# Kernel optimization log

Measured on AMD Instinct MI355X. Metric: run time of the kernel, lower is better.

## Reference

```python
import jax, jax.numpy as jnp
import numpy as np

VOCAB, EMB, HID, LAYERS = 23, 16, 256, 8


def _lstm_layer(xseq, Wih, Whh, bih, bhh):
    # xseq: [B,T,D_in]; Wih: [4H,D_in]; Whh: [4H,H]; biases: [4H]
    B = xseq.shape[0]
    H = Whh.shape[1]
    # precompute input contribution to gates for all timesteps
    xg = jnp.einsum('btd,gd->btg', xseq, Wih) + bih + bhh  # [B,T,4H]
    xg = jnp.swapaxes(xg, 0, 1)  # [T,B,4H] for scan

    def step(carry, g_in):
        h, c = carry
        g = g_in + h @ Whh.T  # [B,4H]
        i, f, gg, o = jnp.split(g, 4, axis=-1)  # PyTorch gate order i,f,g,o
        i = jax.nn.sigmoid(i)
        f = jax.nn.sigmoid(f)
        gg = jnp.tanh(gg)
        o = jax.nn.sigmoid(o)
        c = f * c + i * gg
        h = o * jnp.tanh(c)
        return (h, c), h

    h0 = jnp.zeros((B, H), xseq.dtype)
    c0 = jnp.zeros((B, H), xseq.dtype)
    (_, _), hs = jax.lax.scan(step, (h0, c0), xg)
    return jnp.swapaxes(hs, 0, 1)  # [B,T,H]


def setup_inputs() -> dict:
    key = jax.random.key(0)
    ks = jax.random.split(key, 8)
    B, T = 64, 512
    s_e = 1.0 / np.sqrt(HID)
    x = jax.random.randint(ks[0], (B, T), 0, VOCAB)
    emb = jax.random.normal(ks[1], (VOCAB, EMB), jnp.float32)
    W_ih0 = jax.random.uniform(ks[2], (4 * HID, EMB), jnp.float32, -s_e, s_e)
    W_ih_rest = jax.random.uniform(ks[3], (LAYERS - 1, 4 * HID, HID), jnp.float32, -s_e, s_e)
    W_hh = jax.random.uniform(ks[4], (LAYERS, 4 * HID, HID), jnp.float32, -s_e, s_e)
    b_ih = jax.random.uniform(ks[5], (LAYERS, 4 * HID), jnp.float32, -s_e, s_e)
    b_hh = jax.random.uniform(ks[6], (LAYERS, 4 * HID), jnp.float32, -s_e, s_e)
    fc_w = jax.random.uniform(ks[7], (VOCAB, HID), jnp.float32, -s_e, s_e)
    fc_b = jnp.zeros((VOCAB,), jnp.float32)
    return {"x": x, "emb": emb, "W_ih0": W_ih0, "W_ih_rest": W_ih_rest,
            "W_hh": W_hh, "b_ih": b_ih, "b_hh": b_hh, "fc_w": fc_w, "fc_b": fc_b}


def reference(x, emb, W_ih0, W_ih_rest, W_hh, b_ih, b_hh, fc_w, fc_b):
    h = emb[x]  # [B,T,EMB]
    h = _lstm_layer(h, W_ih0, W_hh[0], b_ih[0], b_hh[0])
    for l in range(1, LAYERS):
        h = _lstm_layer(h, W_ih_rest[l - 1], W_hh[l], b_ih[l], b_hh[l])
    return h @ fc_w.T + fc_b  # [B,T,VOCAB]
```

## Files before the change

### kernel.cpp

```cpp
#include <hip/hip_runtime.h>
#include <cstdint>
#include <cstddef>

#define BB   64
#define TT   512
#define HH   256
#define G4   1024
#define NL   8
#define NW   32
#define HPW  8
#define NR   32

typedef _Float16 half8 __attribute__((ext_vector_type(8)));
typedef float   floatx4 __attribute__((ext_vector_type(4)));

__device__ __forceinline__ float sigm(float v)   { return 1.0f / (1.0f + __expf(-v)); }
__device__ __forceinline__ float tanh_f(float v) { return 1.0f - 2.0f / (__expf(2.0f * v) + 1.0f); }

__device__ __forceinline__ void gload8(half8& d, const _Float16* p) {
  asm volatile("global_load_dwordx4 %0, %1, off sc0 sc1"
               : "=v"(d) : "v"(p) : "memory");
}
__device__ __forceinline__ void gstore8(const _Float16* p, half8 d) {
  asm volatile("global_store_dwordx4 %0, %1, off sc0 sc1"
               :: "v"(p), "v"(d) : "memory");
}
__device__ __forceinline__ void wait_vm0() {
  asm volatile("s_waitcnt vmcnt(0)" ::: "memory");
}

#define TSTRIDE ((size_t)32 * BB * 8)
#define LSTRIDE ((size_t)TT * TSTRIDE)

__global__ void build_xg0(const float* __restrict__ emb, const float* __restrict__ Wih0,
                          float* __restrict__ table) {
  int i = blockIdx.x * 256 + threadIdx.x;
  if (i >= 23 * G4) return;
  int v = i >> 10, n = i & (G4 - 1);
  float a = 0.f;
#pragma unroll
  for (int e = 0; e < 16; ++e) a += emb[v * 16 + e] * Wih0[n * 16 + e];
  table[i] = a;
}

__global__ __launch_bounds__(256, 1) void lstm_pipeline(
    const int*   __restrict__ x,
    const float* __restrict__ Wih_rest,
    const float* __restrict__ Whh,
    const float* __restrict__ bih,
    const float* __restrict__ bhh,
    const float* __restrict__ xg0t,
    _Float16* __restrict__ hseq,
    int* __restrict__ flags)
{
  const int l   = blockIdx.x & 7;
  const int w   = blockIdx.x >> 3;
  const int tid = threadIdx.x;
  const int lane = tid & 63;
  const int p    = tid >> 6;
  const int bb   = tid & 63;

  __shared__ __align__(16) _Float16 wlds[64 * NR * 8];
  __shared__ float  glds[BB * 33];
  __shared__ __align__(16) _Float16 hl[BB * 8];
  __shared__ float  blds[NR];
  __shared__ float  tlds[23 * NR];

  for (int idx = tid; idx < 64 * NR; idx += 256) {
    int kc = idx >> 5;
    int n  = idx & 31;
    int g = n >> 3, jl = n & 7;
    int gr = g * 256 + w * HPW + jl;
    float v[8];
    if (kc < 32) {
      if (l == 0) { for (int j = 0; j < 8; ++j) v[j] = 0.f; }
      else {
        const float* src = Wih_rest + ((size_t)(l - 1) * G4 + gr) * HH + kc * 8;
        for (int j = 0; j < 8; ++j) v[j] = src[j];
      }
    } else {
      const float* src = Whh + ((size_t)l * G4 + gr) * HH + (kc - 32) * 8;
      for (int j = 0; j < 8; ++j) v[j] = src[j];
    }
    _Float16* dst = wlds + (size_t)idx * 8;
    for (int j = 0; j < 8; ++j) dst[j] = (_Float16)v[j];
  }
  if (tid < NR) {
    int g = tid >> 3, jl = tid & 7;
    int gr = g * 256 + w * HPW + jl;
    blds[tid] = bih[l * G4 + gr] + bhh[l * G4 + gr];
  }
  if (l == 0) {
    for (int idx = tid; idx < 23 * NR; idx += 256) {
      int v = idx >> 5, n = idx & 31;
      int g = n >> 3, jl = n & 7;
      tlds[idx] = xg0t[v * G4 + g * 256 + w * HPW + jl];
    }
  }
  __syncthreads();

  float c0 = 0.f, c1 = 0.f;

  const int arow = p * 16 + (lane & 15);
  const int kq   = lane >> 4;
  const int n0   = lane & 15;
  const int n1   = 16 + n0;

  const _Float16* hin  = hseq + (size_t)(l > 0 ? l - 1 : 0) * LSTRIDE;
  _Float16*       hrec = hseq + (size_t)l * LSTRIDE;
  int* flg_in  = flags + (l > 0 ? (l - 1) * TT : 0);
  int* flg_own = flags + l * TT;

  for (int t = 0; t < TT; ++t) {
    floatx4 acc0 = {0.f, 0.f, 0.f, 0.f};
    floatx4 acc1 = {0.f, 0.f, 0.f, 0.f};

    if (tid == 0 && l > 0) {
      while (__hip_atomic_load(flg_in + t, __ATOMIC_RELAXED, __HIP_MEMORY_SCOPE_AGENT) < NW)
        __builtin_amdgcn_s_sleep(1);
    }
    __syncthreads();

    if (l > 0) {
      const _Float16* ain = hin + (size_t)t * TSTRIDE;
      half8 a[8];
#pragma unroll
      for (int kt = 0; kt < 8; ++kt) {
        int kc = kt * 4 + kq;
        gload8(a[kt], ain + ((size_t)(kc * 64 + arow) << 3));
      }
      wait_vm0();
#pragma unroll
      for (int kt = 0; kt < 8; ++kt) {
        int kc = kt * 4 + kq;
        half8 w0 = *(const half8*)(wlds + ((kc * 32 + n0) << 3));
        half8 w1 = *(const half8*)(wlds + ((kc * 32 + n1) << 3));
        acc0 = __builtin_amdgcn_mfma_f32_16x16x32_f16(a[kt], w0, acc0, 0, 0, 0);
        acc1 = __builtin_amdgcn_mfma_f32_16x16x32_f16(a[kt], w1, acc1, 0, 0, 0);
      }
    }

    if (tid == 0 && t > 0) {
      while (__hip_atomic_load(flg_own + (t - 1), __ATOMIC_RELAXED, __HIP_MEMORY_SCOPE_AGENT) < NW)
        __builtin_amdgcn_s_sleep(1);
    }
    __syncthreads();

    if (t > 0) {
      const _Float16* ain = hrec + (size_t)(t - 1) * TSTRIDE;
      half8 a[8];
#pragma unroll
      for (int kt = 0; kt < 8; ++kt) {
        int kc = kt * 4 + kq;
        gload8(a[kt], ain + ((size_t)(kc * 64 + arow) << 3));
      }
      wait_vm0();
#pragma unroll
      for (int kt = 0; kt < 8; ++kt) {
        int kc = kt * 4 + kq;
        half8 w0 = *(const half8*)(wlds + (((32 + kc) * 32 + n0) << 3));
        half8 w1 = *(const half8*)(wlds + (((32 + kc) * 32 + n1) << 3));
        acc0 = __builtin_amdgcn_mfma_f32_16x16x32_f16(a[kt], w0, acc0, 0, 0, 0);
        acc1 = __builtin_amdgcn_mfma_f32_16x16x32_f16(a[kt], w1, acc1, 0, 0, 0);
      }
    }

    {
      int rbase = p * 16 + kq * 4;
#pragma unroll
      for (int r = 0; r < 4; ++r) {
        glds[(rbase + r) * 33 + n0]      = acc0[r];
        glds[(rbase + r) * 33 + 16 + n0] = acc1[r];
      }
    }
    __syncthreads();

    {
      int xv = 0;
      if (l == 0) xv = x[bb * TT + t];
      float h0, h1;
#pragma unroll
      for (int q = 0; q < 2; ++q) {
        int j = 2 * p + q;
        float gi = glds[bb * 33 + j]      + blds[j];
        float gf = glds[bb * 33 + 8 + j]  + blds[8 + j];
        float gg = glds[bb * 33 + 16 + j] + blds[16 + j];
        float go = glds[bb * 33 + 24 + j] + blds[24 + j];
        if (l == 0) {
          const float* tb = tlds + xv * NR;
          gi += tb[j]; gf += tb[8 + j]; gg += tb[16 + j]; go += tb[24 + j];
        }
        float iv = sigm(gi), fv = sigm(gf), gv = tanh_f(gg), ov = sigm(go);
        float cv = (q == 0) ? c0 : c1;
        cv = fv * cv + iv * gv;
        float hv = ov * tanh_f(cv);
        if (q == 0) { c0 = cv; h0 = hv; } else { c1 = cv; h1 = hv; }
      }
      hl[bb * 8 + 2 * p]     = (_Float16)h0;
      hl[bb * 8 + 2 * p + 1] = (_Float16)h1;
    }
    __syncthreads();

    if (tid < 64) {
      half8 hv = *(const half8*)(hl + tid * 8);
      gstore8(hrec + (size_t)t * TSTRIDE + ((size_t)w * 64 + tid) * 8, hv);
      wait_vm0();
      if (tid == 0)
        __hip_atomic_fetch_add(flg_own + t, 1, __ATOMIC_RELAXED, __HIP_MEMORY_SCOPE_AGENT);
    }
  }
}

__global__ __launch_bounds__(256) void fc_kernel(
    const _Float16* __restrict__ hseq7,
    const float* __restrict__ fcw,
    const float* __restrict__ fcb,
    float* __restrict__ out)
{
  const int t = blockIdx.x;
  const int tid = threadIdx.x;
  __shared__ __align__(16) _Float16 hbuf[32 * 64 * 8];
  __shared__ float wbuf[23 * 256];
  __shared__ float bbuf[24];

  const _Float16* src = hseq7 + (size_t)t * TSTRIDE;
  for (int i = tid; i < 32 * 64; i += 256)
    ((half8*)hbuf)[i] = ((const half8*)src)[i];
  for (int i = tid; i < 23 * 256; i += 256) wbuf[i] = fcw[i];
  if (tid < 23) bbuf[tid] = fcb[tid];
  __syncthreads();

  for (int o = tid; o < 64 * 23; o += 256) {
    int b = o / 23, v = o - b * 23;
    float acc = bbuf[v];
#pragma unroll 4
    for (int kc = 0; kc < 32; ++kc) {
      half8 hv = *(const half8*)(hbuf + ((kc * 64 + b) << 3));
      const float* wr = wbuf + v * 256 + kc * 8;
#pragma unroll
      for (int j = 0; j < 8; ++j) acc += (float)hv[j] * wr[j];
    }
    out[((size_t)b * TT + t) * 23 + v] = acc;
  }
}

extern "C" void kernel_launch(void* const* d_in, const int* in_sizes, int n_in,
                              void* d_out, int out_size, void* d_ws, size_t ws_size,
                              hipStream_t stream) {
  const int*   x        = (const int*)d_in[0];
  const float* emb      = (const float*)d_in[1];
  const float* Wih0     = (const float*)d_in[2];
  const float* Wih_rest = (const float*)d_in[3];
  const float* Whh      = (const float*)d_in[4];
  const float* bihp     = (const float*)d_in[5];
  const float* bhhp     = (const float*)d_in[6];
  const float* fcw      = (const float*)d_in[7];
  const float* fcb      = (const float*)d_in[8];
  float* out = (float*)d_out;

  char* ws = (char*)d_ws;
  int*      flags = (int*)ws;
  float*    table = (float*)(ws + 16384);
  _Float16* hseq  = (_Float16*)(ws + 131072);

  hipMemsetAsync(flags, 0, NL * TT * sizeof(int), stream);
  build_xg0<<<(23 * G4 + 255) / 256, 256, 0, stream>>>(emb, Wih0, table);
  lstm_pipeline<<<NL * NW, 256, 0, stream>>>(x, Wih_rest, Whh, bihp, bhhp, table, hseq, flags);
  fc_kernel<<<TT, 256, 0, stream>>>(hseq + (size_t)7 * LSTRIDE, fcw, fcb, out);
}
```

Before: 1.927 ms.

## Replace atomic step counters with per-workgroup progress flags and merged waits

Each workgroup now writes its own progress word (the step index) with a plain store, and does not atomically increment a shared per-step counter. Consumers poll all 32 words with one wavefront-wide load and a vote. The two waits (previous layer, own layer) run in parallel on different waves and are followed by a single barrier, so both input loads are issued together. The h output is now written straight from every thread as dwords, with no LDS staging step, which removes a barrier per step. The cost is more polling traffic and more small global stores. Correctness relies on the sc0 sc1 stores becoming visible before the flag store.

Result: slower. 2.068 ms (+7.3%).

```diff
diff --git a/kernel.cpp b/kernel.cpp
--- a/kernel.cpp
+++ b/kernel.cpp
@@ -17,16 +17,18 @@
 __device__ __forceinline__ float sigm(float v)   { return 1.0f / (1.0f + __expf(-v)); }
 __device__ __forceinline__ float tanh_f(float v) { return 1.0f - 2.0f / (__expf(2.0f * v) + 1.0f); }
 
-__device__ __forceinline__ void gload8(half8& d, const _Float16* p) {
-  asm volatile("global_load_dwordx4 %0, %1, off sc0 sc1"
-               : "=v"(d) : "v"(p) : "memory");
-}
-__device__ __forceinline__ void gstore8(const _Float16* p, half8 d) {
-  asm volatile("global_store_dwordx4 %0, %1, off sc0 sc1"
-               :: "v"(p), "v"(d) : "memory");
+__device__ __forceinline__ void gload8_x(half8& d, const _Float16* p) {
+  asm volatile("global_load_dwordx4 %0, %1, off sc0 sc1" : "=v"(d) : "v"(p) : "memory");
+}
+__device__ __forceinline__ void stdword_x(int* p, int v) {
+  asm volatile("global_store_dword %0, %1, off sc0 sc1" :: "v"(p), "v"(v) : "memory");
 }
 __device__ __forceinline__ void wait_vm0() {
   asm volatile("s_waitcnt vmcnt(0)" ::: "memory");
+}
+__device__ __forceinline__ int ldflag_x(const int* p) {
+  int v; asm volatile("global_load_dword %0, %1, off sc0 sc1" : "=v"(v) : "v"(p) : "memory");
+  wait_vm0(); return v;
 }
 
 #define TSTRIDE ((size_t)32 * BB * 8)
@@ -51,7 +53,7 @@
     const float* __restrict__ bhh,
     const float* __restrict__ xg0t,
     _Float16* __restrict__ hseq,
-    int* __restrict__ flags)
+    int* __restrict__ cnt)
 {
   const int l   = blockIdx.x & 7;
   const int w   = blockIdx.x >> 3;
@@ -62,7 +64,6 @@
 
   __shared__ __align__(16) _Float16 wlds[64 * NR * 8];
   __shared__ float  glds[BB * 33];
-  __shared__ __align__(16) _Float16 hl[BB * 8];
   __shared__ float  blds[NR];
   __shared__ float  tlds[23 * NR];
 
@@ -108,60 +109,65 @@
 
   const _Float16* hin  = hseq + (size_t)(l > 0 ? l - 1 : 0) * LSTRIDE;
   _Float16*       hrec = hseq + (size_t)l * LSTRIDE;
-  int* flg_in  = flags + (l > 0 ? (l - 1) * TT : 0);
-  int* flg_own = flags + l * TT;
 
   for (int t = 0; t < TT; ++t) {
+    if (t > 0 && p == 3) {
+      const int* f = cnt + l * NW;
+      for (;;) {
+        int v = ldflag_x(f + (lane & 31));
+        if (__all(v >= t)) break;
+        __builtin_amdgcn_s_sleep(1);
+      }
+    }
+    if (l > 0 && p == 2) {
+      const int* f = cnt + (l - 1) * NW;
+      for (;;) {
+        int v = ldflag_x(f + (lane & 31));
+        if (__all(v >= t + 1)) break;
+        __builtin_amdgcn_s_sleep(1);
+      }
+    }
+    __syncthreads();
+
+    half8 aA[8], aB[8];
+    if (l > 0) {
+      const _Float16* ain = hin + (size_t)t * TSTRIDE;
+#pragma unroll
+      for (int kt = 0; kt < 8; ++kt) {
+        int kc = kt * 4 + kq;
+        gload8_x(aA[kt], ain + ((size_t)(kc * 64 + arow) << 3));
+      }
+    }
+    if (t > 0) {
+      const _Float16* ain = hrec + (size_t)(t - 1) * TSTRIDE;
+#pragma unroll
+      for (int kt = 0; kt < 8; ++kt) {
+        int kc = kt * 4 + kq;
+        gload8_x(aB[kt], ain + ((size_t)(kc * 64 + arow) << 3));
+      }
+    }
+    wait_vm0();
+
     floatx4 acc0 = {0.f, 0.f, 0.f, 0.f};
     floatx4 acc1 = {0.f, 0.f, 0.f, 0.f};
-
-    if (tid == 0 && l > 0) {
-      while (__hip_atomic_load(flg_in + t, __ATOMIC_RELAXED, __HIP_MEMORY_SCOPE_AGENT) < NW)
-        __builtin_amdgcn_s_sleep(1);
-    }
-    __syncthreads();
-
     if (l > 0) {
-      const _Float16* ain = hin + (size_t)t * TSTRIDE;
-      half8 a[8];
-#pragma unroll
-      for (int kt = 0; kt < 8; ++kt) {
-        int kc = kt * 4 + kq;
-        gload8(a[kt], ain + ((size_t)(kc * 64 + arow) << 3));
-      }
-      wait_vm0();
 #pragma unroll
       for (int kt = 0; kt < 8; ++kt) {
         int kc = kt * 4 + kq;
         half8 w0 = *(const half8*)(wlds + ((kc * 32 + n0) << 3));
         half8 w1 = *(const half8*)(wlds + ((kc * 32 + n1) << 3));
-        acc0 = __builtin_amdgcn_mfma_f32_16x16x32_f16(a[kt], w0, acc0, 0, 0, 0);
-        acc1 = __builtin_amdgcn_mfma_f32_16x16x32_f16(a[kt], w1, acc1, 0, 0, 0);
-      }
-    }
-
-    if (tid == 0 && t > 0) {
-      while (__hip_atomic_load(flg_own + (t - 1), __ATOMIC_RELAXED, __HIP_MEMORY_SCOPE_AGENT) < NW)
-        __builtin_amdgcn_s_sleep(1);
-    }
-    __syncthreads();
-
+        acc0 = __builtin_amdgcn_mfma_f32_16x16x32_f16(aA[kt], w0, acc0, 0, 0, 0);
+        acc1 = __builtin_amdgcn_mfma_f32_16x16x32_f16(aA[kt], w1, acc1, 0, 0, 0);
+      }
+    }
     if (t > 0) {
-      const _Float16* ain = hrec + (size_t)(t - 1) * TSTRIDE;
-      half8 a[8];
-#pragma unroll
-      for (int kt = 0; kt < 8; ++kt) {
-        int kc = kt * 4 + kq;
-        gload8(a[kt], ain + ((size_t)(kc * 64 + arow) << 3));
-      }
-      wait_vm0();
 #pragma unroll
       for (int kt = 0; kt < 8; ++kt) {
         int kc = kt * 4 + kq;
         half8 w0 = *(const half8*)(wlds + (((32 + kc) * 32 + n0) << 3));
         half8 w1 = *(const half8*)(wlds + (((32 + kc) * 32 + n1) << 3));
-        acc0 = __builtin_amdgcn_mfma_f32_16x16x32_f16(a[kt], w0, acc0, 0, 0, 0);
-        acc1 = __builtin_amdgcn_mfma_f32_16x16x32_f16(a[kt], w1, acc1, 0, 0, 0);
+        acc0 = __builtin_amdgcn_mfma_f32_16x16x32_f16(aB[kt], w0, acc0, 0, 0, 0);
+        acc1 = __builtin_amdgcn_mfma_f32_16x16x32_f16(aB[kt], w1, acc1, 0, 0, 0);
       }
     }
 
@@ -175,10 +181,10 @@
     }
     __syncthreads();
 
+    union { _Float16 h[2]; int d; } hu;
     {
       int xv = 0;
       if (l == 0) xv = x[bb * TT + t];
-      float h0, h1;
 #pragma unroll
       for (int q = 0; q < 2; ++q) {
         int j = 2 * p + q;
@@ -194,20 +200,16 @@
         float cv = (q == 0) ? c0 : c1;
         cv = fv * cv + iv * gv;
         float hv = ov * tanh_f(cv);
-        if (q == 0) { c0 = cv; h0 = hv; } else { c1 = cv; h1 = hv; }
-      }
-      hl[bb * 8 + 2 * p]     = (_Float16)h0;
-      hl[bb * 8 + 2 * p + 1] = (_Float16)h1;
-    }
+        if (q == 0) c0 = cv; else c1 = cv;
+        hu.h[q] = (_Float16)hv;
+      }
+    }
+
+    stdword_x((int*)(hrec + (size_t)t * TSTRIDE) + ((w * 64 + bb) << 2) + p, hu.d);
+    wait_vm0();
     __syncthreads();
-
-    if (tid < 64) {
-      half8 hv = *(const half8*)(hl + tid * 8);
-      gstore8(hrec + (size_t)t * TSTRIDE + ((size_t)w * 64 + tid) * 8, hv);
-      wait_vm0();
-      if (tid == 0)
-        __hip_atomic_fetch_add(flg_own + t, 1, __ATOMIC_RELAXED, __HIP_MEMORY_SCOPE_AGENT);
-    }
+    if (tid == 0)
+      stdword_x(cnt + l * NW + w, t + 1);
   }
 }
 
@@ -259,12 +261,12 @@
   float* out = (float*)d_out;
 
   char* ws = (char*)d_ws;
-  int*      flags = (int*)ws;
+  int*      cnt   = (int*)ws;
   float*    table = (float*)(ws + 16384);
   _Float16* hseq  = (_Float16*)(ws + 131072);
 
-  hipMemsetAsync(flags, 0, NL * TT * sizeof(int), stream);
+  hipMemsetAsync(ws, 0, 16384, stream);
   build_xg0<<<(23 * G4 + 255) / 256, 256, 0, stream>>>(emb, Wih0, table);
-  lstm_pipeline<<<NL * NW, 256, 0, stream>>>(x, Wih_rest, Whh, bihp, bhhp, table, hseq, flags);
+  lstm_pipeline<<<NL * NW, 256, 0, stream>>>(x, Wih_rest, Whh, bihp, bhhp, table, hseq, cnt);
   fc_kernel<<<TT, 256, 0, stream>>>(hseq + (size_t)7 * LSTRIDE, fcw, fcb, out);
 }
```
